# Optimization experiments

Measured on AMD Instinct MI355X. Metric: run time of the kernel, lower is better.

The kernel has to match this reference:

```python
import jax, jax.numpy as jnp
import numpy as np

H = 16          # num_heads
D = 64          # head_dim = dim // num_heads
ROPE_THETA = 10000.0
NEG = -1e9


def _rope_angles(n, d):
    # matches get_1d_rotary_pos_embed(head_dim, N): freqs_cis = polar(1, t outer (theta^-(2i/d)))
    inv_freq = 1.0 / (ROPE_THETA ** (jnp.arange(0, d, 2, dtype=jnp.float32) / d))  # [d/2]
    ang = jnp.arange(n, dtype=jnp.float32)[:, None] * inv_freq[None, :]            # [n, d/2]
    return jnp.cos(ang), jnp.sin(ang)


def _apply_rope(x, cos, sin):
    # x: [B,H,N,D]; complex rotation on adjacent pairs (use_real=False semantics)
    x0 = x[..., 0::2]
    x1 = x[..., 1::2]
    # broadcast cos/sin [N, D/2] over batch and heads
    r0 = x0 * cos - x1 * sin
    r1 = x0 * sin + x1 * cos
    return jnp.stack([r0, r1], axis=-1).reshape(x.shape)


def setup_inputs() -> dict:
    key = jax.random.key(0)
    ks = jax.random.split(key, 5)
    B, N, C = 4, 2048, 1024
    s_in = 1.0 / np.sqrt(C)
    return {
        "x": jax.random.normal(ks[0], (B, N, C), dtype=jnp.float32),
        "Wqkv_w": jax.random.normal(ks[1], (3 * C, C), dtype=jnp.float32) * s_in,
        "Wqkv_b": jax.random.normal(ks[2], (3 * C,), dtype=jnp.float32) * 0.01,
        "out_w": jax.random.normal(ks[3], (C, C), dtype=jnp.float32) * s_in,
        "out_b": jax.random.normal(ks[4], (C,), dtype=jnp.float32) * 0.01,
    }


def reference(x, Wqkv_w, Wqkv_b, out_w, out_b):
    B, N, C = x.shape
    scale = D ** -0.5
    # fused QKV projection: [B,N,3C] -> [3,B,H,N,D]
    qkv = (jnp.einsum('bnc,oc->bno', x, Wqkv_w) + Wqkv_b)
    qkv = qkv.reshape(B, N, 3, H, D).transpose(2, 0, 3, 1, 4)
    q, k, v = qkv[0], qkv[1], qkv[2]
    # qk_norm=False -> Identity
    cos, sin = _rope_angles(N, D)
    q = _apply_rope(q, cos, sin)
    k = _apply_rope(k, cos, sin)
    attn = jnp.einsum('bhqd,bhkd->bhqk', q * scale, k)      # [B,H,N,N]
    causal = jnp.triu(jnp.ones((N, N), dtype=bool), k=1)
    attn = jnp.where(causal[None, None], NEG, attn)
    attn = jax.nn.softmax(attn, axis=-1)
    o = jnp.einsum('bhqk,bhkd->bhqd', attn, v)              # [B,H,N,D]
    o = o.transpose(0, 2, 1, 3).reshape(B, N, C)
    return jnp.einsum('bnc,oc->bno', o, out_w) + out_b
```

## Files before the change

kernel.cpp:

```cpp
#include <hip/hip_runtime.h>
#include <hip/hip_bf16.h>

#define DEVI __device__ __forceinline__

typedef __attribute__((ext_vector_type(8))) short short8v;
typedef __attribute__((ext_vector_type(4))) float f32x4;
typedef __attribute__((ext_vector_type(2))) unsigned u32x2;

DEVI short f2bf(float f) {
  __hip_bfloat16 h = __float2bfloat16(f);
  return __builtin_bit_cast(short, h);
}
DEVI float bf2f(short s) {
  unsigned u = ((unsigned)(unsigned short)s) << 16;
  return __builtin_bit_cast(float, u);
}
DEVI unsigned packbf(float a, float b) {
  return (unsigned)(unsigned short)f2bf(a) | ((unsigned)(unsigned short)f2bf(b) << 16);
}
DEVI void gload16(const void* g, void* l) {
  __builtin_amdgcn_global_load_lds((const __attribute__((address_space(1))) void*)g,
                                   (__attribute__((address_space(3))) void*)l, 16, 0, 0);
}
#define MFMA16(a, b, c) __builtin_amdgcn_mfma_f32_16x16x32_bf16((a), (b), (c), 0, 0, 0)


__global__ void cvt_all(const float* __restrict__ x, const float* __restrict__ wq,
                        const float* __restrict__ wo, short* __restrict__ xb,
                        short* __restrict__ wqb, short* __restrict__ wob) {
  int i = blockIdx.x * blockDim.x + threadIdx.x;
  const float* in;
  short* out;
  if (i < 2097152) { in = x; out = xb; }
  else if (i < 2097152 + 786432) { in = wq; out = wqb; i -= 2097152; }
  else { in = wo; out = wob; i -= 2097152 + 786432; }
  float4 v = ((const float4*)in)[i];
  short4 o;
  o.x = f2bf(v.x); o.y = f2bf(v.y); o.z = f2bf(v.z); o.w = f2bf(v.w);
  ((short4*)out)[i] = o;
}

__global__ void rope_table(float2* __restrict__ tbl) {
  int i = blockIdx.x * blockDim.x + threadIdx.x;
  int n = i >> 5, f = i & 31;
  float inv = powf(10000.0f, -(float)f * (1.0f / 32.0f));
  float ang = (float)n * inv;
  tbl[i] = make_float2(cosf(ang), sinf(ang));
}

__global__ void rope_k(short* __restrict__ kk, const float2* __restrict__ tbl) {
  int i = blockIdx.x * blockDim.x + threadIdx.x;
  int row = i >> 3, c8 = i & 7;
  int n = row & 2047;
  short* ad = kk + (size_t)row * 64 + c8 * 8;
  short8v vv = *(short8v*)ad;
  short8v ov;
#pragma unroll
  for (int j = 0; j < 4; ++j) {
    float2 cs = tbl[n * 32 + c8 * 4 + j];
    float x0 = bf2f(vv[2 * j]), x1 = bf2f(vv[2 * j + 1]);
    ov[2 * j]     = f2bf(x0 * cs.x - x1 * cs.y);
    ov[2 * j + 1] = f2bf(x0 * cs.y + x1 * cs.x);
  }
  *(short8v*)ad = ov;
}

template <int EPI>
__global__ __launch_bounds__(256)
void gemm_bt(const short* __restrict__ A, const short* __restrict__ Bw,
             const float* __restrict__ bias,
             short* __restrict__ q, short* __restrict__ k, short* __restrict__ v,
             float* __restrict__ fout, int Mdim, int Ndim, int Kdim) {
  __shared__ __attribute__((aligned(16))) short As[2][128 * 64];
  __shared__ __attribute__((aligned(16))) short Bs[2][128 * 64];
  const int t = threadIdx.x;
  const int lane = t & 63, w = t >> 6;
  const int wr = w >> 1, wc = w & 1;
  const int g = lane >> 4, r16 = lane & 15;
  const int m0 = blockIdx.y * 128, n0 = blockIdx.x * 128;

  int goffs[4], loffs[4];
#pragma unroll
  for (int p = 0; p < 4; ++p) {
    int c = p * 256 + t;
    int row = c >> 3, u = c & 7;
    goffs[p] = row * Kdim + ((u ^ (row & 7)) * 8);
    loffs[p] = c * 16;
  }
  const short* Abase = A + (size_t)m0 * Kdim;
  const short* Bbase = Bw + (size_t)n0 * Kdim;

  auto STAGE = [&](int s, int k0) {
#pragma unroll
    for (int p = 0; p < 4; ++p) {
      gload16(Abase + k0 + goffs[p], (char*)&As[s][0] + loffs[p]);
      gload16(Bbase + k0 + goffs[p], (char*)&Bs[s][0] + loffs[p]);
    }
  };

  f32x4 acc[4][4];
#pragma unroll
  for (int i = 0; i < 4; ++i)
#pragma unroll
    for (int j = 0; j < 4; ++j) acc[i][j] = (f32x4){0.f, 0.f, 0.f, 0.f};

  STAGE(0, 0);
  __syncthreads();

  const int nsteps = Kdim >> 6;
  int cur = 0;
  for (int st = 0; st < nsteps; ++st) {
    if (st + 1 < nsteps) STAGE(cur ^ 1, (st + 1) << 6);
#pragma unroll
    for (int ks = 0; ks < 2; ++ks) {
      short8v af[4], bf[4];
#pragma unroll
      for (int mi = 0; mi < 4; ++mi)
        af[mi] = *(const short8v*)((const char*)&As[cur][0] +
                                   (wr * 64 + mi * 16 + r16) * 128 +
                                   (((ks * 4 + g) ^ (r16 & 7)) << 4));
#pragma unroll
      for (int ni = 0; ni < 4; ++ni)
        bf[ni] = *(const short8v*)((const char*)&Bs[cur][0] +
                                   (wc * 64 + ni * 16 + r16) * 128 +
                                   (((ks * 4 + g) ^ (r16 & 7)) << 4));
#pragma unroll
      for (int mi = 0; mi < 4; ++mi)
#pragma unroll
        for (int ni = 0; ni < 4; ++ni)
          acc[mi][ni] = MFMA16(af[mi], bf[ni], acc[mi][ni]);
    }
    __syncthreads();
    cur ^= 1;
  }

  if (EPI == 0) {
#pragma unroll
    for (int ni = 0; ni < 4; ++ni) {
      int col = n0 + wc * 64 + ni * 16 + r16;
      float bv = bias[col];
      int s = col >> 10, rr = col & 1023, h = rr >> 6, d = rr & 63;
      short* dst = (s == 0) ? q : (s == 1 ? k : v);
      const bool vt = (s == 2);
#pragma unroll
      for (int mi = 0; mi < 4; ++mi) {
        int mrow = m0 + wr * 64 + mi * 16 + g * 4;
#pragma unroll
        for (int r = 0; r < 4; ++r) {
          int m = mrow + r;
          int b = m >> 11, n = m & 2047;
          size_t idx = vt ? ((((size_t)(b * 16 + h)) * 64 + d) * 2048 + n)
                          : ((((size_t)(b * 16 + h)) * 2048 + n) * 64 + d);
          dst[idx] = f2bf(acc[mi][ni][r] + bv);
        }
      }
    }
  } else {
#pragma unroll
    for (int ni = 0; ni < 4; ++ni) {
      int col = n0 + wc * 64 + ni * 16 + r16;
      float bv = bias[col];
#pragma unroll
      for (int mi = 0; mi < 4; ++mi) {
        int mrow = m0 + wr * 64 + mi * 16 + g * 4;
#pragma unroll
        for (int r = 0; r < 4; ++r)
          fout[(size_t)(mrow + r) * Ndim + col] = acc[mi][ni][r] + bv;
      }
    }
  }
}

__global__ __launch_bounds__(256)
void fattn(const short* __restrict__ q, const short* __restrict__ k,
           const short* __restrict__ vT, const float2* __restrict__ tbl,
           short* __restrict__ o) {
  const int bx = blockIdx.x;
  const int qt = 15 - (bx >> 6);
  const int bh = bx & 63;
  const int b = bh >> 4, h = bh & 15;
  const int t = threadIdx.x, lane = t & 63, w = t >> 6;
  const int g = lane >> 4, r16 = lane & 15;

  __shared__ __attribute__((aligned(16))) short Ks[2][64 * 64];
  __shared__ __attribute__((aligned(16))) short Vt[2][64 * 64];
  __shared__ __attribute__((aligned(16))) short Ps[4][2][16 * 72];

  const short* qb = q + (size_t)bh * 2048 * 64;
  const short* kb = k + (size_t)bh * 2048 * 64;
  const short* vb = vT + (size_t)bh * 2048 * 64;

  int koffs[2], voffs[2], loffs[2];
#pragma unroll
  for (int p = 0; p < 2; ++p) {
    int c = p * 256 + t;
    int row = c >> 3, u = c & 7;
    int x8 = (u ^ (row & 7)) * 8;
    koffs[p] = row * 64 + x8;
    voffs[p] = row * 2048 + x8;
    loffs[p] = c * 16;
  }
  auto STAGE = [&](int s, int kt) {
#pragma unroll
    for (int p = 0; p < 2; ++p) {
      gload16(kb + (size_t)kt * 4096 + koffs[p], (char*)&Ks[s][0] + loffs[p]);
      gload16(vb + kt * 64 + voffs[p], (char*)&Vt[s][0] + loffs[p]);
    }
  };

  const int q0 = qt * 128 + w * 32;

  const float sc = 0.125f * 1.44269504088896f;
  short8v aq[2][2];
#pragma unroll
  for (int qi = 0; qi < 2; ++qi) {
    const int n = q0 + qi * 16 + r16;
#pragma unroll
    for (int dk = 0; dk < 2; ++dk) {
      short8v raw = *(const short8v*)(qb + (size_t)n * 64 + dk * 32 + g * 8);
      short8v rq;
#pragma unroll
      for (int j = 0; j < 4; ++j) {
        float2 cs = tbl[n * 32 + dk * 16 + g * 4 + j];
        float x0 = bf2f(raw[2 * j]), x1 = bf2f(raw[2 * j + 1]);
        rq[2 * j]     = f2bf((x0 * cs.x - x1 * cs.y) * sc);
        rq[2 * j + 1] = f2bf((x0 * cs.y + x1 * cs.x) * sc);
      }
      aq[qi][dk] = rq;
    }
  }

  const short one_bf = 0x3F80;
  const short8v ones = {one_bf, one_bf, one_bf, one_bf, one_bf, one_bf, one_bf, one_bf};
  const float M = 24.0f;

  f32x4 oacc[2][4], lacc[2];
#pragma unroll
  for (int qi = 0; qi < 2; ++qi) {
#pragma unroll
    for (int dc = 0; dc < 4; ++dc) oacc[qi][dc] = (f32x4){0.f, 0.f, 0.f, 0.f};
    lacc[qi] = (f32x4){0.f, 0.f, 0.f, 0.f};
  }

  const int ktmax = 2 * qt + 1;

  STAGE(0, 0);
  __syncthreads();

  for (int kt = 0; kt <= ktmax; ++kt) {
    const int cur = kt & 1;
    if (kt < ktmax) STAGE(cur ^ 1, kt + 1);

    const bool act0 = (kt * 64 <= q0 + 15);
    const bool act1 = (kt * 64 <= q0 + 31);

    f32x4 s[2][4];
#pragma unroll
    for (int qi = 0; qi < 2; ++qi)
#pragma unroll
      for (int kc = 0; kc < 4; ++kc) s[qi][kc] = (f32x4){0.f, 0.f, 0.f, 0.f};

    if (act1) {
#pragma unroll
      for (int kc = 0; kc < 4; ++kc) {
        int key = kc * 16 + r16;
        const char* rb = (const char*)&Ks[cur][0] + key * 128;
        short8v kf0 = *(const short8v*)(rb + (((g) ^ (key & 7)) << 4));
        short8v kf1 = *(const short8v*)(rb + (((4 + g) ^ (key & 7)) << 4));
        if (act0) {
          s[0][kc] = MFMA16(kf0, aq[0][0], s[0][kc]);
          s[0][kc] = MFMA16(kf1, aq[0][1], s[0][kc]);
        }
        s[1][kc] = MFMA16(kf0, aq[1][0], s[1][kc]);
        s[1][kc] = MFMA16(kf1, aq[1][1], s[1][kc]);
      }

#pragma unroll
      for (int qi = 0; qi < 2; ++qi) {
        if (qi == 0 && !act0) continue;
        const int qrow = q0 + qi * 16 + r16;
        const bool needmask = (kt * 64 + 63 > q0 + qi * 16);
        if (needmask) {
#pragma unroll
          for (int kc = 0; kc < 4; ++kc)
#pragma unroll
            for (int r = 0; r < 4; ++r)
              if (kt * 64 + kc * 16 + g * 4 + r > qrow) s[qi][kc][r] = -1e30f;
        }
        unsigned pk[4][2];
#pragma unroll
        for (int kc = 0; kc < 4; ++kc) {
          float p0 = __builtin_amdgcn_exp2f(s[qi][kc][0] - M);
          float p1 = __builtin_amdgcn_exp2f(s[qi][kc][1] - M);
          float p2 = __builtin_amdgcn_exp2f(s[qi][kc][2] - M);
          float p3 = __builtin_amdgcn_exp2f(s[qi][kc][3] - M);
          pk[kc][0] = packbf(p0, p1);
          pk[kc][1] = packbf(p2, p3);
        }
#pragma unroll
        for (int kc = 0; kc < 4; ++kc)
          *(u32x2*)((char*)&Ps[w][qi][0] + r16 * 144 + kc * 32 + g * 8) =
              (u32x2){pk[kc][0], pk[kc][1]};
      }

      asm volatile("" ::: "memory");

      short8v pa[2][2];
#pragma unroll
      for (int qi = 0; qi < 2; ++qi) {
        if (qi == 0 && !act0) continue;
#pragma unroll
        for (int kk = 0; kk < 2; ++kk)
          pa[qi][kk] =
              *(const short8v*)((char*)&Ps[w][qi][0] + r16 * 144 + kk * 64 + g * 16);
      }
      if (act0) {
        lacc[0] = MFMA16(pa[0][0], ones, lacc[0]);
        lacc[0] = MFMA16(pa[0][1], ones, lacc[0]);
      }
      lacc[1] = MFMA16(pa[1][0], ones, lacc[1]);
      lacc[1] = MFMA16(pa[1][1], ones, lacc[1]);
#pragma unroll
      for (int dc = 0; dc < 4; ++dc) {
        int d = dc * 16 + r16;
        const char* vr = (const char*)&Vt[cur][0] + d * 128;
#pragma unroll
        for (int kk = 0; kk < 2; ++kk) {
          short8v bv = *(const short8v*)(vr + (((kk * 4 + g) ^ (d & 7)) << 4));
          if (act0) oacc[0][dc] = MFMA16(pa[0][kk], bv, oacc[0][dc]);
          oacc[1][dc] = MFMA16(pa[1][kk], bv, oacc[1][dc]);
        }
      }
    }
    __syncthreads();
  }

#pragma unroll
  for (int qi = 0; qi < 2; ++qi) {
#pragma unroll
    for (int r = 0; r < 4; ++r) {
      float ilr = 1.f / lacc[qi][r];
      int qg = q0 + qi * 16 + g * 4 + r;
      short* orow = o + ((size_t)(b * 2048 + qg)) * 1024 + h * 64;
#pragma unroll
      for (int dc = 0; dc < 4; ++dc)
        orow[dc * 16 + r16] = f2bf(oacc[qi][dc][r] * ilr);
    }
  }
}

extern "C" void kernel_launch(void* const* d_in, const int* in_sizes, int n_in,
                              void* d_out, int out_size, void* d_ws, size_t ws_size,
                              hipStream_t stream) {
  const float* x    = (const float*)d_in[0];
  const float* Wqkv = (const float*)d_in[1];
  const float* bqkv = (const float*)d_in[2];
  const float* Wout = (const float*)d_in[3];
  const float* bout = (const float*)d_in[4];

  char* p = (char*)d_ws;
  short* xb = (short*)p;    p += (size_t)8192 * 1024 * 2;
  short* wqkvb = (short*)p; p += (size_t)3072 * 1024 * 2;
  short* woutb = (short*)p; p += (size_t)1024 * 1024 * 2;
  short* qbf = (short*)p;   p += (size_t)64 * 2048 * 64 * 2;
  short* kbf = (short*)p;   p += (size_t)64 * 2048 * 64 * 2;
  short* vbf = (short*)p;   p += (size_t)64 * 2048 * 64 * 2;
  float2* tbl = (float2*)p; p += (size_t)2048 * 32 * 8;

  cvt_all<<<12288, 256, 0, stream>>>(x, Wqkv, Wout, xb, wqkvb, woutb);
  rope_table<<<256, 256, 0, stream>>>(tbl);

  gemm_bt<0><<<dim3(24, 64), 256, 0, stream>>>(xb, wqkvb, bqkv, qbf, kbf, vbf, nullptr,
                                               8192, 3072, 1024);
  rope_k<<<4096, 256, 0, stream>>>(kbf, tbl);
  fattn<<<dim3(1024), 256, 0, stream>>>(qbf, kbf, vbf, tbl, xb);
  gemm_bt<1><<<dim3(8, 64), 256, 0, stream>>>(xb, woutb, bout, nullptr, nullptr, nullptr,
                                              (float*)d_out, 8192, 1024, 1024);
}
```

Before: 199.3 us.

## Use triple-buffered K=32 LDS pipeline with partial vmcnt waits in GEMM

Changes the projection GEMM from double-buffered 64-wide K tiles to triple-buffered 32-wide K tiles. Two stages are prefetched ahead, and each iteration waits only for the older stage's loads via s_waitcnt vmcnt(4) instead of draining all loads at __syncthreads. The LDS swizzle is adjusted for the 64-byte row width. The aim is to keep more global loads in flight and overlap memory with MFMA, at the cost of twice as many barriers per K and less MFMA work between barriers.

```diff
diff --git a/kernel.cpp b/kernel.cpp
--- a/kernel.cpp
+++ b/kernel.cpp
@@ -71,20 +71,20 @@
              const float* __restrict__ bias,
              short* __restrict__ q, short* __restrict__ k, short* __restrict__ v,
              float* __restrict__ fout, int Mdim, int Ndim, int Kdim) {
-  __shared__ __attribute__((aligned(16))) short As[2][128 * 64];
-  __shared__ __attribute__((aligned(16))) short Bs[2][128 * 64];
+  __shared__ __attribute__((aligned(16))) short As[3][128 * 32];
+  __shared__ __attribute__((aligned(16))) short Bs[3][128 * 32];
   const int t = threadIdx.x;
   const int lane = t & 63, w = t >> 6;
   const int wr = w >> 1, wc = w & 1;
   const int g = lane >> 4, r16 = lane & 15;
   const int m0 = blockIdx.y * 128, n0 = blockIdx.x * 128;
 
-  int goffs[4], loffs[4];
-#pragma unroll
-  for (int p = 0; p < 4; ++p) {
+  int goffs[2], loffs[2];
+#pragma unroll
+  for (int p = 0; p < 2; ++p) {
     int c = p * 256 + t;
-    int row = c >> 3, u = c & 7;
-    goffs[p] = row * Kdim + ((u ^ (row & 7)) * 8);
+    int row = c >> 2, u = c & 3;
+    goffs[p] = row * Kdim + ((u ^ ((row >> 1) & 3)) * 8);
     loffs[p] = c * 16;
   }
   const short* Abase = A + (size_t)m0 * Kdim;
@@ -92,7 +92,7 @@
 
   auto STAGE = [&](int s, int k0) {
 #pragma unroll
-    for (int p = 0; p < 4; ++p) {
+    for (int p = 0; p < 2; ++p) {
       gload16(Abase + k0 + goffs[p], (char*)&As[s][0] + loffs[p]);
       gload16(Bbase + k0 + goffs[p], (char*)&Bs[s][0] + loffs[p]);
     }
@@ -104,34 +104,37 @@
 #pragma unroll
     for (int j = 0; j < 4; ++j) acc[i][j] = (f32x4){0.f, 0.f, 0.f, 0.f};
 
+  const int nsteps = Kdim >> 5;
   STAGE(0, 0);
-  __syncthreads();
-
-  const int nsteps = Kdim >> 6;
-  int cur = 0;
+  STAGE(1, 32);
+  asm volatile("s_waitcnt vmcnt(4)" ::: "memory");
+  __builtin_amdgcn_s_barrier();
+  asm volatile("" ::: "memory");
+
+  int cur = 0, pre = 2;
+  const int rsw = (r16 >> 1) & 3;
   for (int st = 0; st < nsteps; ++st) {
-    if (st + 1 < nsteps) STAGE(cur ^ 1, (st + 1) << 6);
-#pragma unroll
-    for (int ks = 0; ks < 2; ++ks) {
-      short8v af[4], bf[4];
-#pragma unroll
-      for (int mi = 0; mi < 4; ++mi)
-        af[mi] = *(const short8v*)((const char*)&As[cur][0] +
-                                   (wr * 64 + mi * 16 + r16) * 128 +
-                                   (((ks * 4 + g) ^ (r16 & 7)) << 4));
+    if (st + 2 < nsteps) STAGE(pre, (st + 2) << 5);
+    short8v af[4], bf[4];
+#pragma unroll
+    for (int mi = 0; mi < 4; ++mi)
+      af[mi] = *(const short8v*)&As[cur][(wr * 64 + mi * 16 + r16) * 32 +
+                                         ((g ^ rsw) * 8)];
+#pragma unroll
+    for (int ni = 0; ni < 4; ++ni)
+      bf[ni] = *(const short8v*)&Bs[cur][(wc * 64 + ni * 16 + r16) * 32 +
+                                         ((g ^ rsw) * 8)];
+#pragma unroll
+    for (int mi = 0; mi < 4; ++mi)
 #pragma unroll
       for (int ni = 0; ni < 4; ++ni)
-        bf[ni] = *(const short8v*)((const char*)&Bs[cur][0] +
-                                   (wc * 64 + ni * 16 + r16) * 128 +
-                                   (((ks * 4 + g) ^ (r16 & 7)) << 4));
-#pragma unroll
-      for (int mi = 0; mi < 4; ++mi)
-#pragma unroll
-        for (int ni = 0; ni < 4; ++ni)
-          acc[mi][ni] = MFMA16(af[mi], bf[ni], acc[mi][ni]);
-    }
-    __syncthreads();
-    cur ^= 1;
+        acc[mi][ni] = MFMA16(af[mi], bf[ni], acc[mi][ni]);
+    if (st + 2 < nsteps) asm volatile("s_waitcnt vmcnt(4)" ::: "memory");
+    else                 asm volatile("s_waitcnt vmcnt(0)" ::: "memory");
+    __builtin_amdgcn_s_barrier();
+    asm volatile("" ::: "memory");
+    cur = (cur == 2) ? 0 : cur + 1;
+    pre = (pre == 2) ? 0 : pre + 1;
   }
 
   if (EPI == 0) {
```

Result: slower. 206.2 us (+3.5%).
